# Kernel tuning notes

Hardware: AMD Instinct MI355X
Metric: run time of the kernel (lower is better)

## Reference

```python
import jax, jax.numpy as jnp
import numpy as np

D_MODEL = 512
DFF = 2048
E = 8
K = 2
B, N = 2, 2048


def setup_inputs() -> dict:
    key = jax.random.key(0)
    ks = jax.random.split(key, 6)
    x = jax.random.normal(ks[0], (B, N, D_MODEL), dtype=jnp.float32)
    # router: nn.Linear(d_model, E, bias=False), init normal(std=0.01), weight [E, d]
    router_w = jax.random.normal(ks[1], (E, D_MODEL), dtype=jnp.float32) * 0.01
    # expert linear1.weight [dff, d], linear2.weight [d, dff], xavier-uniform; biases zero in torch init,
    # but use small random biases so the backward test exercises their grads meaningfully.
    lim1 = float(np.sqrt(6.0 / (D_MODEL + DFF)))
    w1_all = jax.random.uniform(ks[2], (E, DFF, D_MODEL), minval=-lim1, maxval=lim1, dtype=jnp.float32)
    w2_all = jax.random.uniform(ks[3], (E, D_MODEL, DFF), minval=-lim1, maxval=lim1, dtype=jnp.float32)
    b1_all = jax.random.normal(ks[4], (E, DFF), dtype=jnp.float32) * 0.01
    b2_all = jax.random.normal(ks[5], (E, D_MODEL), dtype=jnp.float32) * 0.01
    return {"x": x, "router_w": router_w, "w1_all": w1_all, "b1_all": b1_all,
            "w2_all": w2_all, "b2_all": b2_all}


def reference(x, router_w, w1_all, b1_all, w2_all, b2_all):
    Bb, Nn, C = x.shape
    L = Bb * Nn
    x_flat = x.reshape(L, C)

    # Router: logits -> softmax -> top-k -> renormalized weights
    router_logits = x_flat @ router_w.T                      # [L, E]
    router_probs = jax.nn.softmax(router_logits, axis=-1)
    expert_weights, expert_indices = jax.lax.top_k(router_probs, K)  # [L, K]
    expert_weights = expert_weights / (jnp.sum(expert_weights, axis=-1, keepdims=True) + 1e-9)

    # Dense per-expert MLP (same math as per-token gathered bmm; dropout in eval = identity)
    h = jax.nn.relu(jnp.einsum('lc,efc->lef', x_flat, w1_all) + b1_all[None])  # [L, E, dff]
    out_all = jnp.einsum('lef,ecf->lec', h, w2_all) + b2_all[None]             # [L, E, C]

    # Gather selected experts' outputs and combine
    out_sel = jnp.take_along_axis(out_all, expert_indices[:, :, None], axis=1)  # [L, K, C]
    final = jnp.sum(out_sel * expert_weights[:, :, None], axis=1)               # [L, C]
    return final.reshape(Bb, Nn, C)
```

## Files before the change

kernel.cpp:

```cpp
#include <hip/hip_runtime.h>

#define D_MODEL 512
#define DFF 2048
#define NEXP 8
#define LTOK 4096
#define NPAIR 8192
#define PMAX 9216
#define MAXT 72

#define HD_COUNTS 0
#define HD_CURSOR 8
#define HD_OFF    16
#define HD_NTILES 25
#define HD_TILE_E 32
#define HD_TILE_R 112

typedef __attribute__((ext_vector_type(8))) short bf16x8;
typedef __attribute__((ext_vector_type(4))) float f32x4;

__device__ __forceinline__ unsigned short f2bf(float f){
  unsigned u = __builtin_bit_cast(unsigned, f);
  u += 0x7fffu + ((u>>16)&1u);
  return (unsigned short)(u>>16);
}

template<int N> __device__ __forceinline__ void wait_vm(){
  if constexpr (N==6)      asm volatile("s_waitcnt vmcnt(6)" ::: "memory");
  else                     asm volatile("s_waitcnt vmcnt(0)" ::: "memory");
}
#define RAW_BARRIER() asm volatile("s_barrier" ::: "memory")

__global__ void prep_kernel(const float* __restrict__ w1, const float* __restrict__ w2,
                            unsigned short* __restrict__ w1b, unsigned short* __restrict__ w2b,
                            const float* __restrict__ x, const float* __restrict__ rw,
                            int* __restrict__ pair_e, float* __restrict__ pair_w){
  int bx = blockIdx.x;
  int tid = threadIdx.x;
  if (bx < 8192){
    int id = bx*256 + tid;
    const int per = NEXP*DFF*D_MODEL/8;
    const float* src; unsigned short* dst; int k;
    if (id < per){ src = w1; dst = w1b; k = id; }
    else         { src = w2; dst = w2b; k = id - per; }
    const float4* s = (const float4*)(src + (size_t)k*8);
    float4 a = s[0], b = s[1];
    uint4 o;
    o.x = (unsigned)f2bf(a.x) | ((unsigned)f2bf(a.y)<<16);
    o.y = (unsigned)f2bf(a.z) | ((unsigned)f2bf(a.w)<<16);
    o.z = (unsigned)f2bf(b.x) | ((unsigned)f2bf(b.y)<<16);
    o.w = (unsigned)f2bf(b.z) | ((unsigned)f2bf(b.w)<<16);
    *(uint4*)(dst + (size_t)k*8) = o;
  } else {
    int t = (bx - 8192)*4 + (tid>>6);
    int l = tid & 63;
    const float* xr = x + (size_t)t*D_MODEL;
    float xv[8];
    #pragma unroll
    for (int j=0;j<8;j++) xv[j] = xr[j*64+l];
    double lg[NEXP];
    #pragma unroll
    for (int e=0;e<NEXP;e++){
      const float* we = rw + e*D_MODEL;
      double s = 0.0;
      #pragma unroll
      for (int j=0;j<8;j++) s += (double)xv[j] * (double)we[j*64+l];
      #pragma unroll
      for (int off=32; off; off>>=1) s += __shfl_xor(s, off);
      lg[e] = s;
    }
    if (l==0){
      double mx = lg[0];
      #pragma unroll
      for (int e=1;e<NEXP;e++) if (lg[e]>mx) mx = lg[e];
      double p[NEXP], sum = 0.0;
      #pragma unroll
      for (int e=0;e<NEXP;e++){ p[e] = exp(lg[e]-mx); sum += p[e]; }
      #pragma unroll
      for (int e=0;e<NEXP;e++) p[e] /= sum;
      int i0 = 0;
      for (int e=1;e<NEXP;e++) if (p[e] > p[i0]) i0 = e;
      int i1 = (i0==0) ? 1 : 0;
      for (int e=0;e<NEXP;e++){ if (e==i0) continue; if (p[e] > p[i1]) i1 = e; }
      double s2 = p[i0] + p[i1] + 1e-9;
      pair_e[2*t]   = i0;  pair_e[2*t+1] = i1;
      pair_w[2*t]   = (float)(p[i0]/s2);
      pair_w[2*t+1] = (float)(p[i1]/s2);
    }
  }
}

__global__ void count_kernel(const int* __restrict__ pair_e, int* __restrict__ hdr){
  __shared__ int cnt[NEXP];
  int tid = threadIdx.x;
  if (tid < NEXP) cnt[tid] = 0;
  __syncthreads();
  int base = blockIdx.x*1024;
  #pragma unroll
  for (int i=0;i<4;i++) atomicAdd(&cnt[pair_e[base + i*256 + tid]], 1);
  __syncthreads();
  if (tid < NEXP) atomicAdd(&hdr[HD_COUNTS+tid], cnt[tid]);
}

__global__ void plan_kernel(int* __restrict__ hdr, int* __restrict__ gtk){
  if (threadIdx.x==0){
    int off=0, nt=0;
    for (int e=0;e<NEXP;e++){
      hdr[HD_OFF+e]=off;
      int c = hdr[HD_COUNTS+e];
      int tiles = (c+127)>>7;
      for (int i=0;i<tiles;i++){ hdr[HD_TILE_E+nt]=e; hdr[HD_TILE_R+nt]=off+(i<<7); nt++; }
      off += tiles<<7;
    }
    hdr[HD_OFF+NEXP]=off;
    hdr[HD_NTILES]=nt;
  }
  for (int i=threadIdx.x; i<PMAX; i+=blockDim.x) gtk[i]=-1;
}

__global__ void assign_gather_kernel(const int* __restrict__ pair_e, int* __restrict__ hdr,
                                     int* __restrict__ gtk, const float* __restrict__ x,
                                     unsigned short* __restrict__ xg){
  __shared__ int cnt[NEXP];
  __shared__ int base[NEXP];
  __shared__ int rowbuf[256];
  int tid = threadIdx.x;
  if (tid < NEXP) cnt[tid] = 0;
  __syncthreads();
  int id = blockIdx.x*256 + tid;
  int e = pair_e[id];
  int myrank = atomicAdd(&cnt[e], 1);
  __syncthreads();
  if (tid < NEXP) base[tid] = atomicAdd(&hdr[HD_CURSOR+tid], cnt[tid]);
  __syncthreads();
  int row = hdr[HD_OFF+e] + base[e] + myrank;
  gtk[row] = id;
  rowbuf[tid] = row;
  __syncthreads();
  int grp = tid>>6, sub = tid&63;
  int base0 = blockIdx.x*256;
  for (int p = grp; p < 256; p += 4){
    int r = rowbuf[p];
    int t = (base0 + p)>>1;
    const float4* s = (const float4*)(x + (size_t)t*D_MODEL + sub*8);
    float4 a = s[0], b = s[1];
    uint4 o;
    o.x = (unsigned)f2bf(a.x) | ((unsigned)f2bf(a.y)<<16);
    o.y = (unsigned)f2bf(a.z) | ((unsigned)f2bf(a.w)<<16);
    o.z = (unsigned)f2bf(b.x) | ((unsigned)f2bf(b.y)<<16);
    o.w = (unsigned)f2bf(b.z) | ((unsigned)f2bf(b.w)<<16);
    *(uint4*)(xg + (size_t)r*D_MODEL + sub*8) = o;
  }
}

__global__ __launch_bounds__(512,2) void gemm1_k(
    const unsigned short* __restrict__ A,
    const unsigned short* __restrict__ Bw,
    const float* __restrict__ bias,
    unsigned short* __restrict__ outH,
    const int* __restrict__ hdr)
{
  constexpr int NWG = MAXT*8;
  __shared__ __align__(16) unsigned short As[2*128*64];
  __shared__ __align__(16) unsigned short Bs[2*256*64];

  int wg  = blockIdx.x;
  int swz = (wg & 7)*(NWG/8) + (wg >> 3);
  int m   = swz >> 3;
  int n0  = (swz & 7) << 8;

  if (m >= hdr[HD_NTILES]) return;
  int e    = hdr[HD_TILE_E+m];
  int row0 = hdr[HD_TILE_R+m];

  int tid = threadIdx.x;
  int w = tid>>6, l = tid&63;
  int wm = w>>2, wn = w&3;

  const unsigned short* Ag = A  + (size_t)row0*D_MODEL;
  const unsigned short* Bg = Bw + (size_t)e*DFF*D_MODEL + (size_t)n0*D_MODEL;

  f32x4 acc[4][4];
  f32x4 zz = {0.f,0.f,0.f,0.f};
  #pragma unroll
  for (int i=0;i<4;i++)
    #pragma unroll
    for (int j=0;j<4;j++) acc[i][j] = zz;

  int srow = (w<<3) + (l>>3);
  int c8   = l&7;
  char* AsB = (char*)As;
  char* BsB = (char*)Bs;

  auto stage = [&](int b, int kt){
    #pragma unroll
    for (int i=0;i<2;i++){
      int r  = i*64 + srow;
      int sc = (c8 ^ (r&7))*8;
      const unsigned short* ga = Ag + (size_t)r*D_MODEL + kt*64 + sc;
      int ldso = b*16384 + i*8192 + w*1024 + l*16;
      __builtin_amdgcn_global_load_lds((const __attribute__((address_space(1))) void*)ga,
                                       (__attribute__((address_space(3))) void*)(AsB + ldso), 16, 0, 0);
    }
    #pragma unroll
    for (int i=0;i<4;i++){
      int r  = i*64 + srow;
      int sc = (c8 ^ (r&7))*8;
      const unsigned short* gb = Bg + (size_t)r*D_MODEL + kt*64 + sc;
      int ldso = b*32768 + i*8192 + w*1024 + l*16;
      __builtin_amdgcn_global_load_lds((const __attribute__((address_space(1))) void*)gb,
                                       (__attribute__((address_space(3))) void*)(BsB + ldso), 16, 0, 0);
    }
  };

  auto compute = [&](int b){
    #pragma unroll
    for (int kk=0;kk<2;kk++){
      bf16x8 av[4], bv[4];
      #pragma unroll
      for (int mi=0;mi<4;mi++){
        int r  = (wm<<6) + (mi<<4) + (l&15);
        int ch = ((kk<<2) + (l>>4)) ^ (r&7);
        av[mi] = *(const bf16x8*)(AsB + b*16384 + r*128 + ch*16);
      }
      #pragma unroll
      for (int ni=0;ni<4;ni++){
        int r  = (wn<<6) + (ni<<4) + (l&15);
        int ch = ((kk<<2) + (l>>4)) ^ (r&7);
        bv[ni] = *(const bf16x8*)(BsB + b*32768 + r*128 + ch*16);
      }
      #pragma unroll
      for (int mi=0;mi<4;mi++)
        #pragma unroll
        for (int ni=0;ni<4;ni++)
          acc[mi][ni] = __builtin_amdgcn_mfma_f32_16x16x32_bf16(av[mi], bv[ni], acc[mi][ni], 0,0,0);
    }
  };

  stage(0, 0);
  int cur = 0;
  for (int kt=0; kt<D_MODEL/64-1; ++kt){
    stage(cur^1, kt+1);
    wait_vm<6>();
    RAW_BARRIER();
    compute(cur);
    asm volatile("s_waitcnt lgkmcnt(0)" ::: "memory");
    RAW_BARRIER();
    cur ^= 1;
  }
  wait_vm<0>();
  RAW_BARRIER();
  compute(cur);

  int lc = l&15, lq = l>>4;
  #pragma unroll
  for (int ni=0;ni<4;ni++){
    int col = n0 + (wn<<6) + (ni<<4) + lc;
    float bcol = bias[e*DFF + col];
    #pragma unroll
    for (int mi=0;mi<4;mi++){
      int rbase = row0 + (wm<<6) + (mi<<4) + lq*4;
      #pragma unroll
      for (int q=0;q<4;q++){
        float v = acc[mi][ni][q] + bcol;
        v = v>0.f ? v : 0.f;
        outH[(size_t)(rbase+q)*DFF + col] = f2bf(v);
      }
    }
  }
}

__global__ __launch_bounds__(256,3) void gemm2_k(
    const unsigned short* __restrict__ A,
    const unsigned short* __restrict__ Bw,
    const float* __restrict__ bias,
    float* __restrict__ outO,
    const float* __restrict__ pair_w,
    const int* __restrict__ hdr,
    const int* __restrict__ gtk)
{
  constexpr int NWG = 2*MAXT*4;
  __shared__ __align__(16) unsigned short As[2*64*64];
  __shared__ __align__(16) unsigned short Bs[2*128*64];

  int wg  = blockIdx.x;
  int swz = (wg & 7)*(NWG/8) + (wg >> 3);
  int m   = swz >> 2;
  int n0  = (swz & 3) << 7;

  if (m >= 2*hdr[HD_NTILES]) return;
  int e    = hdr[HD_TILE_E+(m>>1)];
  int row0 = hdr[HD_TILE_R+(m>>1)] + ((m&1)<<6);

  int tid = threadIdx.x;
  int w = tid>>6, l = tid&63;

  const unsigned short* Ag = A  + (size_t)row0*DFF;
  const unsigned short* Bg = Bw + (size_t)e*D_MODEL*DFF + (size_t)n0*DFF;

  f32x4 acc[4][2];
  f32x4 zz = {0.f,0.f,0.f,0.f};
  #pragma unroll
  for (int i=0;i<4;i++)
    #pragma unroll
    for (int j=0;j<2;j++) acc[i][j] = zz;

  int srow = (w<<3) + (l>>3);
  int c8   = l&7;
  char* AsB = (char*)As;
  char* BsB = (char*)Bs;

  auto stage = [&](int b, int kt){
    #pragma unroll
    for (int i=0;i<2;i++){
      int r  = i*32 + srow;
      int sc = (c8 ^ (r&7))*8;
      const unsigned short* ga = Ag + (size_t)r*DFF + kt*64 + sc;
      int ldso = b*8192 + i*4096 + w*1024 + l*16;
      __builtin_amdgcn_global_load_lds((const __attribute__((address_space(1))) void*)ga,
                                       (__attribute__((address_space(3))) void*)(AsB + ldso), 16, 0, 0);
    }
    #pragma unroll
    for (int i=0;i<4;i++){
      int r  = i*32 + srow;
      int sc = (c8 ^ (r&7))*8;
      const unsigned short* gb = Bg + (size_t)r*DFF + kt*64 + sc;
      int ldso = b*16384 + i*4096 + w*1024 + l*16;
      __builtin_amdgcn_global_load_lds((const __attribute__((address_space(1))) void*)gb,
                                       (__attribute__((address_space(3))) void*)(BsB + ldso), 16, 0, 0);
    }
  };

  auto compute = [&](int b){
    #pragma unroll
    for (int kk=0;kk<2;kk++){
      bf16x8 av[4], bv[2];
      #pragma unroll
      for (int mi=0;mi<4;mi++){
        int r  = (mi<<4) + (l&15);
        int ch = ((kk<<2) + (l>>4)) ^ (r&7);
        av[mi] = *(const bf16x8*)(AsB + b*8192 + r*128 + ch*16);
      }
      #pragma unroll
      for (int ni=0;ni<2;ni++){
        int r  = (w<<5) + (ni<<4) + (l&15);
        int ch = ((kk<<2) + (l>>4)) ^ (r&7);
        bv[ni] = *(const bf16x8*)(BsB + b*16384 + r*128 + ch*16);
      }
      #pragma unroll
      for (int mi=0;mi<4;mi++)
        #pragma unroll
        for (int ni=0;ni<2;ni++)
          acc[mi][ni] = __builtin_amdgcn_mfma_f32_16x16x32_bf16(av[mi], bv[ni], acc[mi][ni], 0,0,0);
    }
  };

  stage(0, 0);
  int cur = 0;
  for (int kt=0; kt<DFF/64-1; ++kt){
    stage(cur^1, kt+1);
    wait_vm<6>();
    RAW_BARRIER();
    compute(cur);
    asm volatile("s_waitcnt lgkmcnt(0)" ::: "memory");
    RAW_BARRIER();
    cur ^= 1;
  }
  wait_vm<0>();
  RAW_BARRIER();
  compute(cur);

  int lc = l&15, lq = l>>4;
  #pragma unroll
  for (int ni=0;ni<2;ni++){
    int col = n0 + (w<<5) + (ni<<4) + lc;
    float bcol = bias[e*D_MODEL + col];
    #pragma unroll
    for (int mi=0;mi<4;mi++){
      int rbase = row0 + (mi<<4) + lq*4;
      #pragma unroll
      for (int q=0;q<4;q++){
        int gr = rbase + q;
        float v = acc[mi][ni][q] + bcol;
        int tk = gtk[gr];
        if (tk>=0){
          float wgt = pair_w[tk];
          atomicAdd(&outO[(size_t)(tk>>1)*D_MODEL + col], wgt*v);
        }
      }
    }
  }
}

extern "C" void kernel_launch(void* const* d_in, const int* in_sizes, int n_in,
                              void* d_out, int out_size, void* d_ws, size_t ws_size,
                              hipStream_t stream){
  const float* x  = (const float*)d_in[0];
  const float* rw = (const float*)d_in[1];
  const float* w1 = (const float*)d_in[2];
  const float* b1 = (const float*)d_in[3];
  const float* w2 = (const float*)d_in[4];
  const float* b2 = (const float*)d_in[5];
  float* out = (float*)d_out;

  const size_t OFF_HDR  = 0;
  const size_t OFF_PE   = 1024;
  const size_t OFF_PW   = 66560;
  const size_t OFF_GTK  = 99328;
  const size_t OFF_XG   = 180224;
  const size_t OFF_W1B  = OFF_XG  + (size_t)PMAX*D_MODEL*2;
  const size_t OFF_W2B  = OFF_W1B + (size_t)NEXP*DFF*D_MODEL*2;
  const size_t OFF_H    = OFF_W2B + (size_t)NEXP*DFF*D_MODEL*2;
  const size_t WS_NEED  = OFF_H   + (size_t)PMAX*DFF*2;
  if (ws_size < WS_NEED) return;

  char* ws = (char*)d_ws;
  int*   hdr    = (int*)(ws + OFF_HDR);
  int*   pair_e = (int*)(ws + OFF_PE);
  float* pair_w = (float*)(ws + OFF_PW);
  int*   gtk    = (int*)(ws + OFF_GTK);
  unsigned short* xg  = (unsigned short*)(ws + OFF_XG);
  unsigned short* w1b = (unsigned short*)(ws + OFF_W1B);
  unsigned short* w2b = (unsigned short*)(ws + OFF_W2B);
  unsigned short* h   = (unsigned short*)(ws + OFF_H);

  hipMemsetAsync(hdr, 0, 1024, stream);
  hipMemsetAsync(out, 0, (size_t)LTOK*D_MODEL*sizeof(float), stream);
  prep_kernel<<<9216, 256, 0, stream>>>(w1, w2, w1b, w2b, x, rw, pair_e, pair_w);
  count_kernel<<<NPAIR/1024, 256, 0, stream>>>(pair_e, hdr);
  plan_kernel<<<1, 256, 0, stream>>>(hdr, gtk);
  assign_gather_kernel<<<NPAIR/256, 256, 0, stream>>>(pair_e, hdr, gtk, x, xg);
  gemm1_k<<<MAXT*8, 512, 0, stream>>>(xg, w1b, b1, h, hdr);
  gemm2_k<<<2*MAXT*4, 256, 0, stream>>>(h, w2b, b2, out, pair_w, hdr, gtk);
}
```

Before: 156.8 us.

## Split-K second GEMM with deterministic combine, retile first GEMM, separate router

Splits the prep kernel into a small router kernel and a weight-conversion kernel. GEMM1 becomes a templated 128x128-tile kernel with 256 threads instead of 128x256 with 512 threads, for more workgroups and better occupancy. When the workspace allows, GEMM2 is split along K into two halves that write fp32 partials, and a combine kernel adds the partials, bias and router weights per token. This removes the output memset and the atomics, at the cost of extra partial-buffer traffic and another launch.

```diff
diff --git a/kernel.cpp b/kernel.cpp
--- a/kernel.cpp
+++ b/kernel.cpp
@@ -25,68 +25,66 @@
 }
 
 template<int N> __device__ __forceinline__ void wait_vm(){
-  if constexpr (N==6)      asm volatile("s_waitcnt vmcnt(6)" ::: "memory");
+  if constexpr (N==8)      asm volatile("s_waitcnt vmcnt(8)" ::: "memory");
+  else if constexpr (N==6) asm volatile("s_waitcnt vmcnt(6)" ::: "memory");
   else                     asm volatile("s_waitcnt vmcnt(0)" ::: "memory");
 }
 #define RAW_BARRIER() asm volatile("s_barrier" ::: "memory")
 
-__global__ void prep_kernel(const float* __restrict__ w1, const float* __restrict__ w2,
-                            unsigned short* __restrict__ w1b, unsigned short* __restrict__ w2b,
-                            const float* __restrict__ x, const float* __restrict__ rw,
+__global__ void router_top2(const float* __restrict__ x, const float* __restrict__ rw,
                             int* __restrict__ pair_e, float* __restrict__ pair_w){
-  int bx = blockIdx.x;
-  int tid = threadIdx.x;
-  if (bx < 8192){
-    int id = bx*256 + tid;
-    const int per = NEXP*DFF*D_MODEL/8;
-    const float* src; unsigned short* dst; int k;
-    if (id < per){ src = w1; dst = w1b; k = id; }
-    else         { src = w2; dst = w2b; k = id - per; }
-    const float4* s = (const float4*)(src + (size_t)k*8);
-    float4 a = s[0], b = s[1];
-    uint4 o;
-    o.x = (unsigned)f2bf(a.x) | ((unsigned)f2bf(a.y)<<16);
-    o.y = (unsigned)f2bf(a.z) | ((unsigned)f2bf(a.w)<<16);
-    o.z = (unsigned)f2bf(b.x) | ((unsigned)f2bf(b.y)<<16);
-    o.w = (unsigned)f2bf(b.z) | ((unsigned)f2bf(b.w)<<16);
-    *(uint4*)(dst + (size_t)k*8) = o;
-  } else {
-    int t = (bx - 8192)*4 + (tid>>6);
-    int l = tid & 63;
-    const float* xr = x + (size_t)t*D_MODEL;
-    float xv[8];
-    #pragma unroll
-    for (int j=0;j<8;j++) xv[j] = xr[j*64+l];
-    double lg[NEXP];
-    #pragma unroll
-    for (int e=0;e<NEXP;e++){
-      const float* we = rw + e*D_MODEL;
-      double s = 0.0;
-      #pragma unroll
-      for (int j=0;j<8;j++) s += (double)xv[j] * (double)we[j*64+l];
-      #pragma unroll
-      for (int off=32; off; off>>=1) s += __shfl_xor(s, off);
-      lg[e] = s;
-    }
-    if (l==0){
-      double mx = lg[0];
-      #pragma unroll
-      for (int e=1;e<NEXP;e++) if (lg[e]>mx) mx = lg[e];
-      double p[NEXP], sum = 0.0;
-      #pragma unroll
-      for (int e=0;e<NEXP;e++){ p[e] = exp(lg[e]-mx); sum += p[e]; }
-      #pragma unroll
-      for (int e=0;e<NEXP;e++) p[e] /= sum;
-      int i0 = 0;
-      for (int e=1;e<NEXP;e++) if (p[e] > p[i0]) i0 = e;
-      int i1 = (i0==0) ? 1 : 0;
-      for (int e=0;e<NEXP;e++){ if (e==i0) continue; if (p[e] > p[i1]) i1 = e; }
-      double s2 = p[i0] + p[i1] + 1e-9;
-      pair_e[2*t]   = i0;  pair_e[2*t+1] = i1;
-      pair_w[2*t]   = (float)(p[i0]/s2);
-      pair_w[2*t+1] = (float)(p[i1]/s2);
-    }
-  }
+  int t = blockIdx.x;
+  int l = threadIdx.x;
+  const float* xr = x + (size_t)t*D_MODEL;
+  float xv[8];
+  #pragma unroll
+  for (int j=0;j<8;j++) xv[j] = xr[j*64+l];
+  double lg[NEXP];
+  #pragma unroll
+  for (int e=0;e<NEXP;e++){
+    const float* we = rw + e*D_MODEL;
+    double s = 0.0;
+    #pragma unroll
+    for (int j=0;j<8;j++) s += (double)xv[j] * (double)we[j*64+l];
+    #pragma unroll
+    for (int off=32; off; off>>=1) s += __shfl_xor(s, off);
+    lg[e] = s;
+  }
+  if (l==0){
+    double mx = lg[0];
+    #pragma unroll
+    for (int e=1;e<NEXP;e++) if (lg[e]>mx) mx = lg[e];
+    double p[NEXP], sum = 0.0;
+    #pragma unroll
+    for (int e=0;e<NEXP;e++){ p[e] = exp(lg[e]-mx); sum += p[e]; }
+    #pragma unroll
+    for (int e=0;e<NEXP;e++) p[e] /= sum;
+    int i0 = 0;
+    for (int e=1;e<NEXP;e++) if (p[e] > p[i0]) i0 = e;
+    int i1 = (i0==0) ? 1 : 0;
+    for (int e=0;e<NEXP;e++){ if (e==i0) continue; if (p[e] > p[i1]) i1 = e; }
+    double s2 = p[i0] + p[i1] + 1e-9;
+    pair_e[2*t]   = i0;  pair_e[2*t+1] = i1;
+    pair_w[2*t]   = (float)(p[i0]/s2);
+    pair_w[2*t+1] = (float)(p[i1]/s2);
+  }
+}
+
+__global__ void convw_kernel(const float* __restrict__ w1, const float* __restrict__ w2,
+                             unsigned short* __restrict__ w1b, unsigned short* __restrict__ w2b){
+  int id = blockIdx.x*256 + threadIdx.x;
+  const int per = NEXP*DFF*D_MODEL/8;
+  const float* src; unsigned short* dst; int k;
+  if (id < per){ src = w1; dst = w1b; k = id; }
+  else         { src = w2; dst = w2b; k = id - per; }
+  const float4* s = (const float4*)(src + (size_t)k*8);
+  float4 a = s[0], b = s[1];
+  uint4 o;
+  o.x = (unsigned)f2bf(a.x) | ((unsigned)f2bf(a.y)<<16);
+  o.y = (unsigned)f2bf(a.z) | ((unsigned)f2bf(a.w)<<16);
+  o.z = (unsigned)f2bf(b.x) | ((unsigned)f2bf(b.y)<<16);
+  o.w = (unsigned)f2bf(b.z) | ((unsigned)f2bf(b.w)<<16);
+  *(uint4*)(dst + (size_t)k*8) = o;
 }
 
 __global__ void count_kernel(const int* __restrict__ pair_e, int* __restrict__ hdr){
@@ -118,7 +116,8 @@
 }
 
 __global__ void assign_gather_kernel(const int* __restrict__ pair_e, int* __restrict__ hdr,
-                                     int* __restrict__ gtk, const float* __restrict__ x,
+                                     int* __restrict__ gtk, int* __restrict__ pr,
+                                     const float* __restrict__ x,
                                      unsigned short* __restrict__ xg){
   __shared__ int cnt[NEXP];
   __shared__ int base[NEXP];
@@ -134,6 +133,7 @@
   __syncthreads();
   int row = hdr[HD_OFF+e] + base[e] + myrank;
   gtk[row] = id;
+  pr[id]   = row;
   rowbuf[tid] = row;
   __syncthreads();
   int grp = tid>>6, sub = tid&63;
@@ -152,39 +152,58 @@
   }
 }
 
-__global__ __launch_bounds__(512,2) void gemm1_k(
+template<int MT, int NDIM, int KDIM, int MODE>
+__global__ __launch_bounds__(256,2) void gemm2p(
     const unsigned short* __restrict__ A,
     const unsigned short* __restrict__ Bw,
     const float* __restrict__ bias,
     unsigned short* __restrict__ outH,
-    const int* __restrict__ hdr)
+    float* __restrict__ outO,
+    const float* __restrict__ pair_w,
+    const int* __restrict__ hdr,
+    const int* __restrict__ gtk)
 {
-  constexpr int NWG = MAXT*8;
-  __shared__ __align__(16) unsigned short As[2*128*64];
-  __shared__ __align__(16) unsigned short Bs[2*256*64];
+  constexpr int NT_N = NDIM/128;
+  constexpr int MAXM = (MT==128) ? MAXT : 2*MAXT;
+  constexpr int NWG  = MAXM*NT_N;
+  constexpr int WC   = (MT==128) ? 64 : 32;
+  constexpr int FN   = WC/16;
+  constexpr int LPT  = MT/32 + 4;
+  constexpr int ABYT = MT*128;
+  constexpr int NTK  = KDIM/64;
+
+  __shared__ __align__(16) unsigned short As[2*MT*64];
+  __shared__ __align__(16) unsigned short Bs[2*128*64];
 
   int wg  = blockIdx.x;
   int swz = (wg & 7)*(NWG/8) + (wg >> 3);
-  int m   = swz >> 3;
-  int n0  = (swz & 7) << 8;
-
-  if (m >= hdr[HD_NTILES]) return;
-  int e    = hdr[HD_TILE_E+m];
-  int row0 = hdr[HD_TILE_R+m];
+  int m   = swz / NT_N;
+  int n0  = (swz % NT_N) << 7;
+
+  int ntiles = hdr[HD_NTILES];
+  int e, row0;
+  if constexpr (MT==128){
+    if (m >= ntiles) return;
+    e = hdr[HD_TILE_E+m];  row0 = hdr[HD_TILE_R+m];
+  } else {
+    if (m >= 2*ntiles) return;
+    e = hdr[HD_TILE_E+(m>>1)];  row0 = hdr[HD_TILE_R+(m>>1)] + ((m&1)<<6);
+  }
 
   int tid = threadIdx.x;
   int w = tid>>6, l = tid&63;
-  int wm = w>>2, wn = w&3;
-
-  const unsigned short* Ag = A  + (size_t)row0*D_MODEL;
-  const unsigned short* Bg = Bw + (size_t)e*DFF*D_MODEL + (size_t)n0*D_MODEL;
-
-  f32x4 acc[4][4];
+  int wm = (MT==128) ? (w>>1) : 0;
+  int wn = (MT==128) ? (w&1)  : w;
+
+  const unsigned short* Ag = A  + (size_t)row0*KDIM;
+  const unsigned short* Bg = Bw + (size_t)e*NDIM*KDIM + (size_t)n0*KDIM;
+
+  f32x4 acc[4][FN];
   f32x4 zz = {0.f,0.f,0.f,0.f};
   #pragma unroll
   for (int i=0;i<4;i++)
     #pragma unroll
-    for (int j=0;j<4;j++) acc[i][j] = zz;
+    for (int j=0;j<FN;j++) acc[i][j] = zz;
 
   int srow = (w<<3) + (l>>3);
   int c8   = l&7;
@@ -193,20 +212,20 @@
 
   auto stage = [&](int b, int kt){
     #pragma unroll
-    for (int i=0;i<2;i++){
-      int r  = i*64 + srow;
+    for (int i=0;i<MT/32;i++){
+      int r  = i*32 + srow;
       int sc = (c8 ^ (r&7))*8;
-      const unsigned short* ga = Ag + (size_t)r*D_MODEL + kt*64 + sc;
-      int ldso = b*16384 + i*8192 + w*1024 + l*16;
+      const unsigned short* ga = Ag + (size_t)r*KDIM + kt*64 + sc;
+      int ldso = b*ABYT + i*4096 + w*1024 + l*16;
       __builtin_amdgcn_global_load_lds((const __attribute__((address_space(1))) void*)ga,
                                        (__attribute__((address_space(3))) void*)(AsB + ldso), 16, 0, 0);
     }
     #pragma unroll
     for (int i=0;i<4;i++){
-      int r  = i*64 + srow;
+      int r  = i*32 + srow;
       int sc = (c8 ^ (r&7))*8;
-      const unsigned short* gb = Bg + (size_t)r*D_MODEL + kt*64 + sc;
-      int ldso = b*32768 + i*8192 + w*1024 + l*16;
+      const unsigned short* gb = Bg + (size_t)r*KDIM + kt*64 + sc;
+      int ldso = b*16384 + i*4096 + w*1024 + l*16;
       __builtin_amdgcn_global_load_lds((const __attribute__((address_space(1))) void*)gb,
                                        (__attribute__((address_space(3))) void*)(BsB + ldso), 16, 0, 0);
     }
@@ -215,30 +234,157 @@
   auto compute = [&](int b){
     #pragma unroll
     for (int kk=0;kk<2;kk++){
-      bf16x8 av[4], bv[4];
+      bf16x8 av[4], bv[FN];
       #pragma unroll
       for (int mi=0;mi<4;mi++){
         int r  = (wm<<6) + (mi<<4) + (l&15);
         int ch = ((kk<<2) + (l>>4)) ^ (r&7);
-        av[mi] = *(const bf16x8*)(AsB + b*16384 + r*128 + ch*16);
+        av[mi] = *(const bf16x8*)(AsB + b*ABYT + r*128 + ch*16);
       }
       #pragma unroll
-      for (int ni=0;ni<4;ni++){
-        int r  = (wn<<6) + (ni<<4) + (l&15);
+      for (int ni=0;ni<FN;ni++){
+        int r  = wn*WC + (ni<<4) + (l&15);
         int ch = ((kk<<2) + (l>>4)) ^ (r&7);
-        bv[ni] = *(const bf16x8*)(BsB + b*32768 + r*128 + ch*16);
+        bv[ni] = *(const bf16x8*)(BsB + b*16384 + r*128 + ch*16);
       }
       #pragma unroll
       for (int mi=0;mi<4;mi++)
         #pragma unroll
-        for (int ni=0;ni<4;ni++)
+        for (int ni=0;ni<FN;ni++)
           acc[mi][ni] = __builtin_amdgcn_mfma_f32_16x16x32_bf16(av[mi], bv[ni], acc[mi][ni], 0,0,0);
     }
   };
 
   stage(0, 0);
   int cur = 0;
-  for (int kt=0; kt<D_MODEL/64-1; ++kt){
+  for (int kt=0; kt<NTK-1; ++kt){
+    stage(cur^1, kt+1);
+    wait_vm<LPT>();
+    RAW_BARRIER();
+    compute(cur);
+    asm volatile("s_waitcnt lgkmcnt(0)" ::: "memory");
+    RAW_BARRIER();
+    cur ^= 1;
+  }
+  wait_vm<0>();
+  RAW_BARRIER();
+  compute(cur);
+
+  int lc = l&15, lq = l>>4;
+  #pragma unroll
+  for (int ni=0;ni<FN;ni++){
+    int col = n0 + wn*WC + (ni<<4) + lc;
+    float bcol = bias[e*NDIM + col];
+    #pragma unroll
+    for (int mi=0;mi<4;mi++){
+      int rbase = row0 + (wm<<6) + (mi<<4) + lq*4;
+      #pragma unroll
+      for (int q=0;q<4;q++){
+        int gr = rbase + q;
+        float v = acc[mi][ni][q] + bcol;
+        if (MODE==0){
+          v = v>0.f ? v : 0.f;
+          outH[(size_t)gr*NDIM + col] = f2bf(v);
+        } else {
+          int tk = gtk[gr];
+          if (tk>=0){
+            float wgt = pair_w[tk];
+            atomicAdd(&outO[(size_t)(tk>>1)*D_MODEL + col], wgt*v);
+          }
+        }
+      }
+    }
+  }
+}
+
+__global__ __launch_bounds__(256,3) void gemm2s_k(
+    const unsigned short* __restrict__ A,
+    const unsigned short* __restrict__ Bw,
+    float* __restrict__ P,
+    const int* __restrict__ hdr)
+{
+  constexpr int NWG = 2*MAXT*4*2;
+  constexpr int NTK = 16;
+  __shared__ __align__(16) unsigned short As[2*64*64];
+  __shared__ __align__(16) unsigned short Bs[2*128*64];
+
+  int wg  = blockIdx.x;
+  int swz = (wg & 7)*(NWG/8) + (wg >> 3);
+  int m   = swz >> 3;
+  int nt  = (swz >> 1) & 3;
+  int kh  = swz & 1;
+
+  if (m >= 2*hdr[HD_NTILES]) return;
+  int e    = hdr[HD_TILE_E+(m>>1)];
+  int row0 = hdr[HD_TILE_R+(m>>1)] + ((m&1)<<6);
+  int n0   = nt << 7;
+
+  int tid = threadIdx.x;
+  int w = tid>>6, l = tid&63;
+
+  const unsigned short* Ag = A  + (size_t)row0*DFF + (size_t)kh*1024;
+  const unsigned short* Bg = Bw + (size_t)e*D_MODEL*DFF + (size_t)n0*DFF + (size_t)kh*1024;
+
+  f32x4 acc[4][2];
+  f32x4 zz = {0.f,0.f,0.f,0.f};
+  #pragma unroll
+  for (int i=0;i<4;i++)
+    #pragma unroll
+    for (int j=0;j<2;j++) acc[i][j] = zz;
+
+  int srow = (w<<3) + (l>>3);
+  int c8   = l&7;
+  char* AsB = (char*)As;
+  char* BsB = (char*)Bs;
+
+  auto stage = [&](int b, int kt){
+    #pragma unroll
+    for (int i=0;i<2;i++){
+      int r  = i*32 + srow;
+      int sc = (c8 ^ (r&7))*8;
+      const unsigned short* ga = Ag + (size_t)r*DFF + kt*64 + sc;
+      int ldso = b*8192 + i*4096 + w*1024 + l*16;
+      __builtin_amdgcn_global_load_lds((const __attribute__((address_space(1))) void*)ga,
+                                       (__attribute__((address_space(3))) void*)(AsB + ldso), 16, 0, 0);
+    }
+    #pragma unroll
+    for (int i=0;i<4;i++){
+      int r  = i*32 + srow;
+      int sc = (c8 ^ (r&7))*8;
+      const unsigned short* gb = Bg + (size_t)r*DFF + kt*64 + sc;
+      int ldso = b*16384 + i*4096 + w*1024 + l*16;
+      __builtin_amdgcn_global_load_lds((const __attribute__((address_space(1))) void*)gb,
+                                       (__attribute__((address_space(3))) void*)(BsB + ldso), 16, 0, 0);
+    }
+  };
+
+  auto compute = [&](int b){
+    #pragma unroll
+    for (int kk=0;kk<2;kk++){
+      bf16x8 av[4], bv[2];
+      #pragma unroll
+      for (int mi=0;mi<4;mi++){
+        int r  = (mi<<4) + (l&15);
+        int ch = ((kk<<2) + (l>>4)) ^ (r&7);
+        av[mi] = *(const bf16x8*)(AsB + b*8192 + r*128 + ch*16);
+      }
+      #pragma unroll
+      for (int ni=0;ni<2;ni++){
+        int r  = (w<<5) + (ni<<4) + (l&15);
+        int ch = ((kk<<2) + (l>>4)) ^ (r&7);
+        bv[ni] = *(const bf16x8*)(BsB + b*16384 + r*128 + ch*16);
+      }
+      #pragma unroll
+      for (int mi=0;mi<4;mi++)
+        #pragma unroll
+        for (int ni=0;ni<2;ni++)
+          acc[mi][ni] = __builtin_amdgcn_mfma_f32_16x16x32_bf16(av[mi], bv[ni], acc[mi][ni], 0,0,0);
+    }
+  };
+
+  stage(0, 0);
+  int cur = 0;
+  for (int kt=0; kt<NTK-1; ++kt){
     stage(cur^1, kt+1);
     wait_vm<6>();
     RAW_BARRIER();
@@ -251,144 +397,42 @@
   RAW_BARRIER();
   compute(cur);
 
-  int lc = l&15, lq = l>>4;
-  #pragma unroll
-  for (int ni=0;ni<4;ni++){
-    int col = n0 + (wn<<6) + (ni<<4) + lc;
-    float bcol = bias[e*DFF + col];
-    #pragma unroll
-    for (int mi=0;mi<4;mi++){
-      int rbase = row0 + (wm<<6) + (mi<<4) + lq*4;
-      #pragma unroll
-      for (int q=0;q<4;q++){
-        float v = acc[mi][ni][q] + bcol;
-        v = v>0.f ? v : 0.f;
-        outH[(size_t)(rbase+q)*DFF + col] = f2bf(v);
-      }
-    }
-  }
-}
-
-__global__ __launch_bounds__(256,3) void gemm2_k(
-    const unsigned short* __restrict__ A,
-    const unsigned short* __restrict__ Bw,
-    const float* __restrict__ bias,
-    float* __restrict__ outO,
-    const float* __restrict__ pair_w,
-    const int* __restrict__ hdr,
-    const int* __restrict__ gtk)
-{
-  constexpr int NWG = 2*MAXT*4;
-  __shared__ __align__(16) unsigned short As[2*64*64];
-  __shared__ __align__(16) unsigned short Bs[2*128*64];
-
-  int wg  = blockIdx.x;
-  int swz = (wg & 7)*(NWG/8) + (wg >> 3);
-  int m   = swz >> 2;
-  int n0  = (swz & 3) << 7;
-
-  if (m >= 2*hdr[HD_NTILES]) return;
-  int e    = hdr[HD_TILE_E+(m>>1)];
-  int row0 = hdr[HD_TILE_R+(m>>1)] + ((m&1)<<6);
-
-  int tid = threadIdx.x;
-  int w = tid>>6, l = tid&63;
-
-  const unsigned short* Ag = A  + (size_t)row0*DFF;
-  const unsigned short* Bg = Bw + (size_t)e*D_MODEL*DFF + (size_t)n0*DFF;
-
-  f32x4 acc[4][2];
-  f32x4 zz = {0.f,0.f,0.f,0.f};
-  #pragma unroll
-  for (int i=0;i<4;i++)
-    #pragma unroll
-    for (int j=0;j<2;j++) acc[i][j] = zz;
-
-  int srow = (w<<3) + (l>>3);
-  int c8   = l&7;
-  char* AsB = (char*)As;
-  char* BsB = (char*)Bs;
-
-  auto stage = [&](int b, int kt){
-    #pragma unroll
-    for (int i=0;i<2;i++){
-      int r  = i*32 + srow;
-      int sc = (c8 ^ (r&7))*8;
-      const unsigned short* ga = Ag + (size_t)r*DFF + kt*64 + sc;
-      int ldso = b*8192 + i*4096 + w*1024 + l*16;
-      __builtin_amdgcn_global_load_lds((const __attribute__((address_space(1))) void*)ga,
-                                       (__attribute__((address_space(3))) void*)(AsB + ldso), 16, 0, 0);
-    }
-    #pragma unroll
-    for (int i=0;i<4;i++){
-      int r  = i*32 + srow;
-      int sc = (c8 ^ (r&7))*8;
-      const unsigned short* gb = Bg + (size_t)r*DFF + kt*64 + sc;
-      int ldso = b*16384 + i*4096 + w*1024 + l*16;
-      __builtin_amdgcn_global_load_lds((const __attribute__((address_space(1))) void*)gb,
-                                       (__attribute__((address_space(3))) void*)(BsB + ldso), 16, 0, 0);
-    }
-  };
-
-  auto compute = [&](int b){
-    #pragma unroll
-    for (int kk=0;kk<2;kk++){
-      bf16x8 av[4], bv[2];
-      #pragma unroll
-      for (int mi=0;mi<4;mi++){
-        int r  = (mi<<4) + (l&15);
-        int ch = ((kk<<2) + (l>>4)) ^ (r&7);
-        av[mi] = *(const bf16x8*)(AsB + b*8192 + r*128 + ch*16);
-      }
-      #pragma unroll
-      for (int ni=0;ni<2;ni++){
-        int r  = (w<<5) + (ni<<4) + (l&15);
-        int ch = ((kk<<2) + (l>>4)) ^ (r&7);
-        bv[ni] = *(const bf16x8*)(BsB + b*16384 + r*128 + ch*16);
-      }
-      #pragma unroll
-      for (int mi=0;mi<4;mi++)
-        #pragma unroll
-        for (int ni=0;ni<2;ni++)
-          acc[mi][ni] = __builtin_amdgcn_mfma_f32_16x16x32_bf16(av[mi], bv[ni], acc[mi][ni], 0,0,0);
-    }
-  };
-
-  stage(0, 0);
-  int cur = 0;
-  for (int kt=0; kt<DFF/64-1; ++kt){
-    stage(cur^1, kt+1);
-    wait_vm<6>();
-    RAW_BARRIER();
-    compute(cur);
-    asm volatile("s_waitcnt lgkmcnt(0)" ::: "memory");
-    RAW_BARRIER();
-    cur ^= 1;
-  }
-  wait_vm<0>();
-  RAW_BARRIER();
-  compute(cur);
-
+  float* Pk = P + (size_t)kh*PMAX*D_MODEL;
   int lc = l&15, lq = l>>4;
   #pragma unroll
   for (int ni=0;ni<2;ni++){
     int col = n0 + (w<<5) + (ni<<4) + lc;
-    float bcol = bias[e*D_MODEL + col];
     #pragma unroll
     for (int mi=0;mi<4;mi++){
       int rbase = row0 + (mi<<4) + lq*4;
       #pragma unroll
-      for (int q=0;q<4;q++){
-        int gr = rbase + q;
-        float v = acc[mi][ni][q] + bcol;
-        int tk = gtk[gr];
-        if (tk>=0){
-          float wgt = pair_w[tk];
-          atomicAdd(&outO[(size_t)(tk>>1)*D_MODEL + col], wgt*v);
-        }
-      }
-    }
-  }
+      for (int q=0;q<4;q++)
+        Pk[(size_t)(rbase+q)*D_MODEL + col] = acc[mi][ni][q];
+    }
+  }
+}
+
+__global__ void combine_kernel(const float* __restrict__ P, const int* __restrict__ pr,
+                               const int* __restrict__ pair_e, const float* __restrict__ pair_w,
+                               const float* __restrict__ b2, float* __restrict__ out){
+  int id = blockIdx.x*256 + threadIdx.x;
+  int t = id>>7, c = (id&127)*4;
+  int r0 = pr[2*t], r1 = pr[2*t+1];
+  int e0 = pair_e[2*t], e1 = pair_e[2*t+1];
+  float w0 = pair_w[2*t], w1 = pair_w[2*t+1];
+  const float* P1 = P + (size_t)PMAX*D_MODEL;
+  float4 a0 = *(const float4*)(P  + (size_t)r0*D_MODEL + c);
+  float4 a1 = *(const float4*)(P1 + (size_t)r0*D_MODEL + c);
+  float4 c0 = *(const float4*)(P  + (size_t)r1*D_MODEL + c);
+  float4 c1 = *(const float4*)(P1 + (size_t)r1*D_MODEL + c);
+  float4 bb0 = *(const float4*)(b2 + (size_t)e0*D_MODEL + c);
+  float4 bb1 = *(const float4*)(b2 + (size_t)e1*D_MODEL + c);
+  float4 r;
+  r.x = w0*(a0.x+a1.x+bb0.x) + w1*(c0.x+c1.x+bb1.x);
+  r.y = w0*(a0.y+a1.y+bb0.y) + w1*(c0.y+c1.y+bb1.y);
+  r.z = w0*(a0.z+a1.z+bb0.z) + w1*(c0.z+c1.z+bb1.z);
+  r.w = w0*(a0.w+a1.w+bb0.w) + w1*(c0.w+c1.w+bb1.w);
+  *(float4*)(out + (size_t)t*D_MODEL + c) = r;
 }
 
 extern "C" void kernel_launch(void* const* d_in, const int* in_sizes, int n_in,
@@ -406,29 +450,41 @@
   const size_t OFF_PE   = 1024;
   const size_t OFF_PW   = 66560;
   const size_t OFF_GTK  = 99328;
+  const size_t OFF_PR   = 143360;
   const size_t OFF_XG   = 180224;
   const size_t OFF_W1B  = OFF_XG  + (size_t)PMAX*D_MODEL*2;
   const size_t OFF_W2B  = OFF_W1B + (size_t)NEXP*DFF*D_MODEL*2;
   const size_t OFF_H    = OFF_W2B + (size_t)NEXP*DFF*D_MODEL*2;
-  const size_t WS_NEED  = OFF_H   + (size_t)PMAX*DFF*2;
-  if (ws_size < WS_NEED) return;
+  const size_t WS_BASE  = OFF_H   + (size_t)PMAX*DFF*2;
+  const size_t OFF_P    = WS_BASE;
+  const size_t WS_SPLIT = OFF_P + (size_t)2*PMAX*D_MODEL*4;
+  if (ws_size < WS_BASE) return;
+  bool split = (ws_size >= WS_SPLIT);
 
   char* ws = (char*)d_ws;
   int*   hdr    = (int*)(ws + OFF_HDR);
   int*   pair_e = (int*)(ws + OFF_PE);
   float* pair_w = (float*)(ws + OFF_PW);
   int*   gtk    = (int*)(ws + OFF_GTK);
+  int*   pr     = (int*)(ws + OFF_PR);
   unsigned short* xg  = (unsigned short*)(ws + OFF_XG);
   unsigned short* w1b = (unsigned short*)(ws + OFF_W1B);
   unsigned short* w2b = (unsigned short*)(ws + OFF_W2B);
   unsigned short* h   = (unsigned short*)(ws + OFF_H);
+  float*          P   = (float*)(ws + OFF_P);
 
   hipMemsetAsync(hdr, 0, 1024, stream);
-  hipMemsetAsync(out, 0, (size_t)LTOK*D_MODEL*sizeof(float), stream);
-  prep_kernel<<<9216, 256, 0, stream>>>(w1, w2, w1b, w2b, x, rw, pair_e, pair_w);
+  router_top2<<<LTOK, 64, 0, stream>>>(x, rw, pair_e, pair_w);
+  convw_kernel<<<8192, 256, 0, stream>>>(w1, w2, w1b, w2b);
   count_kernel<<<NPAIR/1024, 256, 0, stream>>>(pair_e, hdr);
   plan_kernel<<<1, 256, 0, stream>>>(hdr, gtk);
-  assign_gather_kernel<<<NPAIR/256, 256, 0, stream>>>(pair_e, hdr, gtk, x, xg);
-  gemm1_k<<<MAXT*8, 512, 0, stream>>>(xg, w1b, b1, h, hdr);
-  gemm2_k<<<2*MAXT*4, 256, 0, stream>>>(h, w2b, b2, out, pair_w, hdr, gtk);
-}
+  assign_gather_kernel<<<NPAIR/256, 256, 0, stream>>>(pair_e, hdr, gtk, pr, x, xg);
+  gemm2p<128, DFF, D_MODEL, 0><<<MAXT*16, 256, 0, stream>>>(xg, w1b, b1, h, nullptr, nullptr, hdr, gtk);
+  if (split){
+    gemm2s_k<<<2*MAXT*4*2, 256, 0, stream>>>(h, w2b, P, hdr);
+    combine_kernel<<<(LTOK*128)/256, 256, 0, stream>>>(P, pr, pair_e, pair_w, b2, out);
+  } else {
+    hipMemsetAsync(out, 0, (size_t)LTOK*D_MODEL*sizeof(float), stream);
+    gemm2p<64, D_MODEL, DFF, 1><<<2*MAXT*4, 256, 0, stream>>>(h, w2b, b2, nullptr, out, pair_w, hdr, gtk);
+  }
+}
```

Measured after the change: 132.5 us. 1.18x faster.
